# Optimization experiments

Hardware: AMD Instinct MI355X
Metric: run time of the kernel (lower is better)

## Reference

```python
import jax, jax.numpy as jnp
import numpy as np

N_NODES = 1000000
N_EDGES = 2000000
N_FEAT = 11          # QM9 num_features
HIDDEN = 64
N_CLASSES = 19       # QM9 num_classes
BATCH = 128


def setup_inputs() -> dict:
    key = jax.random.key(0)
    k = jax.random.split(key, 8)
    x = jax.random.normal(k[0], (N_NODES, N_FEAT), dtype=jnp.float32)
    edge_index = jax.random.randint(k[1], (2, N_EDGES), 0, N_NODES, dtype=jnp.int64)
    y = jax.random.normal(k[2], (BATCH, N_CLASSES), dtype=jnp.float32)
    batch = jnp.sort(jax.random.randint(k[3], (N_NODES,), 0, BATCH, dtype=jnp.int64))
    # GCNConv params: weight [in, hidden], bias [hidden]
    W_conv = jax.random.normal(k[4], (N_FEAT, HIDDEN), dtype=jnp.float32) / np.sqrt(N_FEAT)
    b_conv = jnp.zeros((HIDDEN,), dtype=jnp.float32)
    # Final linear: [hidden, classes]
    W_lin = jax.random.normal(k[5], (HIDDEN, N_CLASSES), dtype=jnp.float32) / np.sqrt(HIDDEN)
    b_lin = jnp.zeros((N_CLASSES,), dtype=jnp.float32)
    return {"x": x, "edge_index": edge_index, "y": y, "batch": batch,
            "W_conv": W_conv, "b_conv": b_conv, "W_lin": W_lin, "b_lin": b_lin}


def reference(x, edge_index, y, batch, W_conv, b_conv, W_lin, b_lin):
    row, col = edge_index[0], edge_index[1]  # source -> target
    # GCN symmetric normalization (add_self_loops=False): deg over targets
    ones = jnp.ones((edge_index.shape[1],), dtype=x.dtype)
    deg = jax.ops.segment_sum(ones, col, num_segments=N_NODES)
    dinv = jnp.where(deg > 0, jax.lax.rsqrt(jnp.maximum(deg, 1.0)), 0.0)
    norm = dinv[row] * dinv[col]  # [E]
    # Transform then aggregate: gather at source, scatter-add at target
    xw = x @ W_conv                                    # [N, H]
    msgs = xw[row] * norm[:, None]                     # [E, H]
    agg = jax.ops.segment_sum(msgs, col, num_segments=N_NODES) + b_conv
    h = jax.nn.relu(agg)                               # [N, H]
    # global_mean_pool over batch ids (size=BATCH)
    summed = jax.ops.segment_sum(h, batch, num_segments=BATCH)   # [B, H]
    counts = jax.ops.segment_sum(jnp.ones((N_NODES,), dtype=x.dtype), batch, num_segments=BATCH)
    pooled = summed / jnp.maximum(counts, 1.0)[:, None]
    # dropout p=0.5 is identity in eval mode
    return pooled @ W_lin + b_lin                      # [B, classes]
```

## Files before the change

kernel.cpp:

```cpp
#include <hip/hip_runtime.h>

#define N_NODES   1000000
#define N_EDGES   2000000
#define N_FEAT    11
#define HIDDEN    64
#define BATCH     128
#define N_CLASSES 19

#define NPB     2048
#define NBUCK   489
#define BCAP    5120
#define EPB     8192
#define PBLK    245
#define NSLOT   8
#define NCHUNK  3907
#define FROW    24
#define ZOFF    (256 * FROW)

typedef __attribute__((ext_vector_type(8))) short v8s;
typedef __attribute__((ext_vector_type(4))) float v4f;

__device__ __forceinline__ unsigned f2b(float v) {
    unsigned u = __float_as_uint(v);
    return (u + 0x7FFFu + ((u >> 16) & 1u)) >> 16;
}

__global__ __launch_bounds__(1024) void part_kernel(const int* __restrict__ row,
                                                    const int* __restrict__ col,
                                                    int* __restrict__ bcnt,
                                                    int* __restrict__ part) {
    __shared__ int lh[512];
    const int t = threadIdx.x;
    if (t < 512) lh[t] = 0;
    __syncthreads();
    const int q0 = (blockIdx.x * EPB) >> 2;
    const int4* col4 = (const int4*)col;
    const int4* row4 = (const int4*)row;
    const int qa = q0 + t, qb = q0 + 1024 + t;
    const bool va = qa < N_EDGES / 4, vb = qb < N_EDGES / 4;
    int4 ca, ra, cb, rb;
    if (va) { ca = col4[qa]; ra = row4[qa]; }
    if (vb) { cb = col4[qb]; rb = row4[qb]; }
    if (va) {
        atomicAdd(&lh[ca.x >> 11], 1); atomicAdd(&lh[ca.y >> 11], 1);
        atomicAdd(&lh[ca.z >> 11], 1); atomicAdd(&lh[ca.w >> 11], 1);
    }
    if (vb) {
        atomicAdd(&lh[cb.x >> 11], 1); atomicAdd(&lh[cb.y >> 11], 1);
        atomicAdd(&lh[cb.z >> 11], 1); atomicAdd(&lh[cb.w >> 11], 1);
    }
    __syncthreads();
    if (t < NBUCK) {
        int v = lh[t];
        if (v) lh[t] = t * BCAP + atomicAdd(&bcnt[t], v);
    }
    __syncthreads();
    int p;
    if (va) {
        p = atomicAdd(&lh[ca.x >> 11], 1); part[p] = (ra.x << 11) | (ca.x & (NPB - 1));
        p = atomicAdd(&lh[ca.y >> 11], 1); part[p] = (ra.y << 11) | (ca.y & (NPB - 1));
        p = atomicAdd(&lh[ca.z >> 11], 1); part[p] = (ra.z << 11) | (ca.z & (NPB - 1));
        p = atomicAdd(&lh[ca.w >> 11], 1); part[p] = (ra.w << 11) | (ca.w & (NPB - 1));
    }
    if (vb) {
        p = atomicAdd(&lh[cb.x >> 11], 1); part[p] = (rb.x << 11) | (cb.x & (NPB - 1));
        p = atomicAdd(&lh[cb.y >> 11], 1); part[p] = (rb.y << 11) | (cb.y & (NPB - 1));
        p = atomicAdd(&lh[cb.z >> 11], 1); part[p] = (rb.z << 11) | (cb.z & (NPB - 1));
        p = atomicAdd(&lh[cb.w >> 11], 1); part[p] = (rb.w << 11) | (cb.w & (NPB - 1));
    }
}

__global__ __launch_bounds__(1024) void sort2_kernel(const int* __restrict__ part,
                                                     const int* __restrict__ bcnt,
                                                     const float* __restrict__ x,
                                                     int* __restrict__ srcs,
                                                     int* __restrict__ nstart,
                                                     unsigned short* __restrict__ ndeg,
                                                     float* __restrict__ dinv,
                                                     unsigned short* __restrict__ xs) {
    __shared__ int cnt[NPB];
    __shared__ int off[NPB];
    __shared__ int tsum[1024];
    __shared__ int stage[BCAP];
    __shared__ int outb[BCAP];
    const int t = threadIdx.x, b = blockIdx.x;
    for (int i = t; i < NPB; i += 1024) cnt[i] = 0;
    __syncthreads();
    const int s0 = b * BCAP, m = bcnt[b];
    for (int j = t; j < m; j += 1024) {
        int v = part[s0 + j];
        stage[j] = v;
        atomicAdd(&cnt[v & (NPB - 1)], 1);
    }
    __syncthreads();
    const int i0 = t * 2;
    int c0 = cnt[i0], c1 = cnt[i0 + 1];
    int s = c0 + c1;
    tsum[t] = s;
    __syncthreads();
    for (int o = 1; o < 1024; o <<= 1) {
        int a = (t >= o) ? tsum[t - o] : 0;
        __syncthreads();
        tsum[t] += a;
        __syncthreads();
    }
    int run = tsum[t] - s;
    off[i0] = run; off[i0 + 1] = run + c0;
    __syncthreads();
    for (int i = t; i < NPB; i += 1024) {
        int n = b * NPB + i;
        if (n < N_NODES) {
            int d = cnt[i];
            float dv = d ? rsqrtf((float)d) : 0.0f;
            dinv[n]   = dv;
            ndeg[n]   = (unsigned short)d;
            nstart[n] = s0 + off[i];
            const float* xr = x + (size_t)n * N_FEAT;
            unsigned h[11];
#pragma unroll
            for (int k = 0; k < 11; ++k) h[k] = f2b(dv * xr[k]);
            uint4 A, B;
            A.x = h[0] | (h[1] << 16); A.y = h[2] | (h[3] << 16);
            A.z = h[4] | (h[5] << 16); A.w = h[6] | (h[7] << 16);
            B.x = h[8] | (h[9] << 16); B.y = h[10]; B.z = 0u; B.w = 0u;
            uint4* o = (uint4*)(xs + (size_t)n * 16);
            o[0] = A; o[1] = B;
        }
    }
    __syncthreads();
    for (int j = t; j < m; j += 1024) {
        int p  = stage[j];
        int cl = p & (NPB - 1);
        int pos = atomicAdd(&off[cl], 1);
        outb[pos] = p >> 11;
    }
    __syncthreads();
    const int m4 = m >> 2;
    int4* d4 = (int4*)(srcs + s0);
    const int4* s4 = (const int4*)outb;
    for (int j = t; j < m4; j += 1024) d4[j] = s4[j];
    for (int j = (m4 << 2) + t; j < m; j += 1024) srcs[s0 + j] = outb[j];
}

__global__ __launch_bounds__(256) void gather_pool_kernel(
    const int* __restrict__ srcs, const unsigned short* __restrict__ xs,
    const int* __restrict__ nstart, const unsigned short* __restrict__ ndeg,
    const float* __restrict__ dinv, const int* __restrict__ batch,
    const float* __restrict__ Wc, const float* __restrict__ bc,
    float* __restrict__ pooled, float* __restrict__ countsf) {
    __shared__ unsigned short fb16[ZOFF + 8];
    __shared__ int   sj0[256];
    __shared__ int   sdeg[256];
    __shared__ float sdinv[256];
    __shared__ int   sbid[256];
    __shared__ int   sperm[256];
    __shared__ int   dcnt[32];
    __shared__ int   doff[32];
    __shared__ float pbuf[2 * HIDDEN];
    __shared__ int   pcnt[NSLOT];
    const int t = threadIdx.x, lane = t & 63, w = t >> 6;
    const int quad = lane >> 4;
    const int base = blockIdx.x * 256;
    {
        int n = base + t;
        bool v = n < N_NODES;
        sj0[t]   = v ? nstart[n] : 0;
        sdeg[t]  = v ? (int)ndeg[n] : 0;
        sdinv[t] = v ? dinv[n] : 0.0f;
        sbid[t]  = v ? batch[n] : -1;
    }
    if (t < 2 * HIDDEN) pbuf[t] = 0.0f;
    if (t < NSLOT) pcnt[t] = 0;
    if (t < 32)    dcnt[t] = 0;
    if (t < 4)     ((unsigned*)(fb16 + ZOFF))[t] = 0u;
    __syncthreads();
    const int bid0 = sbid[0];
    {
        int bid = sbid[t];
        if (bid >= 0) {
            int slot = bid - bid0;
            if (slot >= 0 && slot < NSLOT) atomicAdd(&pcnt[slot], 1);
            else atomicAdd(&countsf[bid], 1.0f);
        }
    }
    int mybin = sdeg[t] < 31 ? sdeg[t] : 31;
    atomicAdd(&dcnt[mybin], 1);
    __syncthreads();
    if (t < 32) {
        int r = 0;
        for (int i = 0; i < t; ++i) r += dcnt[i];
        doff[t] = r;
    }
    __syncthreads();
    int pos = atomicAdd(&doff[mybin], 1);
    sperm[pos] = t;
    __syncthreads();

    {
        int i  = sperm[t];
        int j0 = sj0[i], d = sdeg[i];
        const int e = j0 + d;
        float acc[11];
#pragma unroll
        for (int k = 0; k < 11; ++k) acc[k] = 0.0f;
        for (int j = j0; j < e; j += 4) {
            int j1 = (j + 1 < e) ? j + 1 : j;
            int j2 = (j + 2 < e) ? j + 2 : j;
            int j3 = (j + 3 < e) ? j + 3 : j;
            int r0 = srcs[j], r1 = srcs[j1], r2 = srcs[j2], r3 = srcs[j3];
            const uint4* p0 = (const uint4*)(xs + (size_t)r0 * 16);
            const uint4* p1 = (const uint4*)(xs + (size_t)r1 * 16);
            const uint4* p2 = (const uint4*)(xs + (size_t)r2 * 16);
            const uint4* p3 = (const uint4*)(xs + (size_t)r3 * 16);
            uint4 A0 = p0[0]; uint2 B0 = *(const uint2*)(p0 + 1);
            uint4 A1 = p1[0]; uint2 B1 = *(const uint2*)(p1 + 1);
            uint4 A2 = p2[0]; uint2 B2 = *(const uint2*)(p2 + 1);
            uint4 A3 = p3[0]; uint2 B3 = *(const uint2*)(p3 + 1);
            float m1 = (j + 1 < e) ? 1.0f : 0.0f;
            float m2 = (j + 2 < e) ? 1.0f : 0.0f;
            float m3 = (j + 3 < e) ? 1.0f : 0.0f;
#define ACCF(idx, expr0, expr1, expr2, expr3)                     \
            acc[idx] += __uint_as_float(expr0);                   \
            acc[idx] = fmaf(m1, __uint_as_float(expr1), acc[idx]);\
            acc[idx] = fmaf(m2, __uint_as_float(expr2), acc[idx]);\
            acc[idx] = fmaf(m3, __uint_as_float(expr3), acc[idx]);
            ACCF(0,  A0.x << 16,        A1.x << 16,        A2.x << 16,        A3.x << 16)
            ACCF(1,  A0.x & 0xFFFF0000u, A1.x & 0xFFFF0000u, A2.x & 0xFFFF0000u, A3.x & 0xFFFF0000u)
            ACCF(2,  A0.y << 16,        A1.y << 16,        A2.y << 16,        A3.y << 16)
            ACCF(3,  A0.y & 0xFFFF0000u, A1.y & 0xFFFF0000u, A2.y & 0xFFFF0000u, A3.y & 0xFFFF0000u)
            ACCF(4,  A0.z << 16,        A1.z << 16,        A2.z << 16,        A3.z << 16)
            ACCF(5,  A0.z & 0xFFFF0000u, A1.z & 0xFFFF0000u, A2.z & 0xFFFF0000u, A3.z & 0xFFFF0000u)
            ACCF(6,  A0.w << 16,        A1.w << 16,        A2.w << 16,        A3.w << 16)
            ACCF(7,  A0.w & 0xFFFF0000u, A1.w & 0xFFFF0000u, A2.w & 0xFFFF0000u, A3.w & 0xFFFF0000u)
            ACCF(8,  B0.x << 16,        B1.x << 16,        B2.x << 16,        B3.x << 16)
            ACCF(9,  B0.x & 0xFFFF0000u, B1.x & 0xFFFF0000u, B2.x & 0xFFFF0000u, B3.x & 0xFFFF0000u)
            ACCF(10, B0.y << 16,        B1.y << 16,        B2.y << 16,        B3.y << 16)
#undef ACCF
        }
        unsigned hb[11];
#pragma unroll
        for (int k = 0; k < 11; ++k) hb[k] = f2b(acc[k]);
        uint4 U0, U1;
        U0.x = hb[0] | (hb[1] << 16); U0.y = hb[2]  | (hb[3] << 16);
        U0.z = hb[4] | (hb[5] << 16); U0.w = hb[6]  | (hb[7] << 16);
        U1.x = hb[8] | (hb[9] << 16); U1.y = hb[10]; U1.z = 0u; U1.w = 0u;
        uint4* wp = (uint4*)(fb16 + i * FROW);
        wp[0] = U0; wp[1] = U1;
    }
    __syncthreads();

    const int nch = w * 16 + (lane & 15);
    union { v8s v; unsigned short us[8]; } bf;
#pragma unroll
    for (int j = 0; j < 8; ++j) {
        int k = quad * 8 + j;
        bf.us[j] = (k < 11) ? (unsigned short)f2b(Wc[k * HIDDEN + nch]) : (unsigned short)0;
    }
    const float bias_lane = bc[nch];
    float acc0 = 0.0f, acc1 = 0.0f;
#pragma unroll 4
    for (int mtile = 0; mtile < 16; ++mtile) {
        const v8s* ap = (quad < 2)
            ? (const v8s*)(fb16 + (mtile * 16 + (lane & 15)) * FROW + quad * 8)
            : (const v8s*)(fb16 + ZOFF);
        v8s a = *ap;
        v4f d = __builtin_amdgcn_mfma_f32_16x16x32_bf16(a, bf.v, (v4f){0.f, 0.f, 0.f, 0.f}, 0, 0, 0);
#pragma unroll
        for (int r = 0; r < 4; ++r) {
            int node = mtile * 16 + quad * 4 + r;
            int bid  = sbid[node];
            if (bid >= 0) {
                float h = fmaxf(fmaf(sdinv[node], d[r], bias_lane), 0.0f);
                int slot = bid - bid0;
                if (slot == 0)      acc0 += h;
                else if (slot == 1) acc1 += h;
                else atomicAdd(&pooled[(size_t)bid * HIDDEN + nch], h);
            }
        }
    }
    atomicAdd(&pbuf[nch], acc0);
    atomicAdd(&pbuf[HIDDEN + nch], acc1);
    __syncthreads();
    for (int s = w; s < 2; s += 4) {
        int c = pcnt[s];
        if (c > 0) {
            atomicAdd(&pooled[(size_t)(bid0 + s) * HIDDEN + lane], pbuf[s * HIDDEN + lane]);
            if (lane == 0) atomicAdd(&countsf[bid0 + s], (float)c);
        }
    }
}

__global__ void final_kernel(const float* __restrict__ pooled, const float* __restrict__ counts,
                             const float* __restrict__ Wl, const float* __restrict__ bl,
                             float* __restrict__ out) {
    int i = blockIdx.x * blockDim.x + threadIdx.x;
    if (i >= BATCH * N_CLASSES) return;
    int b = i / N_CLASSES;
    int c = i - b * N_CLASSES;
    float inv = 1.0f / fmaxf(counts[b], 1.0f);
    float s = bl[c];
#pragma unroll 8
    for (int h = 0; h < HIDDEN; ++h)
        s = fmaf(pooled[b * HIDDEN + h] * inv, Wl[h * N_CLASSES + c], s);
    out[i] = s;
}

extern "C" void kernel_launch(void* const* d_in, const int* in_sizes, int n_in,
                              void* d_out, int out_size, void* d_ws, size_t ws_size,
                              hipStream_t stream) {
    const float* x     = (const float*)d_in[0];
    const int*   ei    = (const int*)d_in[1];
    const int*   batch = (const int*)d_in[3];
    const float* Wc    = (const float*)d_in[4];
    const float* bc    = (const float*)d_in[5];
    const float* Wl    = (const float*)d_in[6];
    const float* bl    = (const float*)d_in[7];
    float*       out   = (float*)d_out;

    int*            bcnt    = (int*)d_ws;
    float*          pooled  = (float*)(bcnt + 512);
    float*          countsf = pooled + BATCH * HIDDEN;
    unsigned short* xs      = (unsigned short*)(countsf + BATCH);
    int*            nstart  = (int*)(xs + (size_t)N_NODES * 16);
    unsigned short* ndeg    = (unsigned short*)(nstart + N_NODES);
    float*          dinv    = (float*)(ndeg + N_NODES);
    int*            part    = (int*)(dinv + N_NODES);
    int*            srcs    = part + (size_t)NBUCK * BCAP;

    size_t zero_bytes = (512 + BATCH * HIDDEN + BATCH) * 4;
    hipMemsetAsync(d_ws, 0, zero_bytes, stream);

    const int* row = ei;
    const int* col = ei + N_EDGES;

    part_kernel <<<PBLK, 1024, 0, stream>>>(row, col, bcnt, part);
    sort2_kernel<<<NBUCK, 1024, 0, stream>>>(part, bcnt, x, srcs, nstart, ndeg, dinv, xs);
    gather_pool_kernel<<<NCHUNK, 256, 0, stream>>>(srcs, xs, nstart, ndeg, dinv,
                                                   batch, Wc, bc, pooled, countsf);
    final_kernel<<<(BATCH * N_CLASSES + 255) / 256, 256, 0, stream>>>(pooled, countsf, Wl, bl, out);
}
```

Measured before the change: 213.3 us.

## Fuse memset, partition and bucket sort into one cooperative kernel

```diff
diff --git a/kernel.cpp b/kernel.cpp
--- a/kernel.cpp
+++ b/kernel.cpp
@@ -1,4 +1,7 @@
 #include <hip/hip_runtime.h>
+#include <hip/hip_cooperative_groups.h>
+
+namespace cg = cooperative_groups;
 
 #define N_NODES   1000000
 #define N_EDGES   2000000
@@ -12,6 +15,7 @@
 #define BCAP    5120
 #define EPB     8192
 #define PBLK    245
+#define GPREP   256
 #define NSLOT   8
 #define NCHUNK  3907
 #define FROW    24
@@ -25,121 +29,130 @@
     return (u + 0x7FFFu + ((u >> 16) & 1u)) >> 16;
 }
 
-__global__ __launch_bounds__(1024) void part_kernel(const int* __restrict__ row,
-                                                    const int* __restrict__ col,
-                                                    int* __restrict__ bcnt,
-                                                    int* __restrict__ part) {
-    __shared__ int lh[512];
-    const int t = threadIdx.x;
-    if (t < 512) lh[t] = 0;
-    __syncthreads();
-    const int q0 = (blockIdx.x * EPB) >> 2;
-    const int4* col4 = (const int4*)col;
-    const int4* row4 = (const int4*)row;
-    const int qa = q0 + t, qb = q0 + 1024 + t;
-    const bool va = qa < N_EDGES / 4, vb = qb < N_EDGES / 4;
-    int4 ca, ra, cb, rb;
-    if (va) { ca = col4[qa]; ra = row4[qa]; }
-    if (vb) { cb = col4[qb]; rb = row4[qb]; }
-    if (va) {
-        atomicAdd(&lh[ca.x >> 11], 1); atomicAdd(&lh[ca.y >> 11], 1);
-        atomicAdd(&lh[ca.z >> 11], 1); atomicAdd(&lh[ca.w >> 11], 1);
-    }
-    if (vb) {
-        atomicAdd(&lh[cb.x >> 11], 1); atomicAdd(&lh[cb.y >> 11], 1);
-        atomicAdd(&lh[cb.z >> 11], 1); atomicAdd(&lh[cb.w >> 11], 1);
-    }
-    __syncthreads();
-    if (t < NBUCK) {
-        int v = lh[t];
-        if (v) lh[t] = t * BCAP + atomicAdd(&bcnt[t], v);
-    }
-    __syncthreads();
-    int p;
-    if (va) {
-        p = atomicAdd(&lh[ca.x >> 11], 1); part[p] = (ra.x << 11) | (ca.x & (NPB - 1));
-        p = atomicAdd(&lh[ca.y >> 11], 1); part[p] = (ra.y << 11) | (ca.y & (NPB - 1));
-        p = atomicAdd(&lh[ca.z >> 11], 1); part[p] = (ra.z << 11) | (ca.z & (NPB - 1));
-        p = atomicAdd(&lh[ca.w >> 11], 1); part[p] = (ra.w << 11) | (ca.w & (NPB - 1));
-    }
-    if (vb) {
-        p = atomicAdd(&lh[cb.x >> 11], 1); part[p] = (rb.x << 11) | (cb.x & (NPB - 1));
-        p = atomicAdd(&lh[cb.y >> 11], 1); part[p] = (rb.y << 11) | (cb.y & (NPB - 1));
-        p = atomicAdd(&lh[cb.z >> 11], 1); part[p] = (rb.z << 11) | (cb.z & (NPB - 1));
-        p = atomicAdd(&lh[cb.w >> 11], 1); part[p] = (rb.w << 11) | (cb.w & (NPB - 1));
-    }
-}
-
-__global__ __launch_bounds__(1024) void sort2_kernel(const int* __restrict__ part,
-                                                     const int* __restrict__ bcnt,
-                                                     const float* __restrict__ x,
-                                                     int* __restrict__ srcs,
-                                                     int* __restrict__ nstart,
-                                                     unsigned short* __restrict__ ndeg,
-                                                     float* __restrict__ dinv,
-                                                     unsigned short* __restrict__ xs) {
+__global__ __launch_bounds__(1024) void prep_kernel(
+    const int* __restrict__ row, const int* __restrict__ col,
+    const float* __restrict__ x,
+    int* __restrict__ bcnt, int* __restrict__ part, int* __restrict__ srcs,
+    int* __restrict__ nstart, unsigned short* __restrict__ ndeg,
+    float* __restrict__ dinv, unsigned short* __restrict__ xs,
+    float* __restrict__ pooled, float* __restrict__ countsf) {
+    cg::grid_group grid = cg::this_grid();
     __shared__ int cnt[NPB];
     __shared__ int off[NPB];
     __shared__ int tsum[1024];
     __shared__ int stage[BCAP];
     __shared__ int outb[BCAP];
-    const int t = threadIdx.x, b = blockIdx.x;
-    for (int i = t; i < NPB; i += 1024) cnt[i] = 0;
-    __syncthreads();
-    const int s0 = b * BCAP, m = bcnt[b];
-    for (int j = t; j < m; j += 1024) {
-        int v = part[s0 + j];
-        stage[j] = v;
-        atomicAdd(&cnt[v & (NPB - 1)], 1);
-    }
-    __syncthreads();
-    const int i0 = t * 2;
-    int c0 = cnt[i0], c1 = cnt[i0 + 1];
-    int s = c0 + c1;
-    tsum[t] = s;
-    __syncthreads();
-    for (int o = 1; o < 1024; o <<= 1) {
-        int a = (t >= o) ? tsum[t - o] : 0;
-        __syncthreads();
-        tsum[t] += a;
-        __syncthreads();
-    }
-    int run = tsum[t] - s;
-    off[i0] = run; off[i0 + 1] = run + c0;
-    __syncthreads();
-    for (int i = t; i < NPB; i += 1024) {
-        int n = b * NPB + i;
-        if (n < N_NODES) {
-            int d = cnt[i];
-            float dv = d ? rsqrtf((float)d) : 0.0f;
-            dinv[n]   = dv;
-            ndeg[n]   = (unsigned short)d;
-            nstart[n] = s0 + off[i];
-            const float* xr = x + (size_t)n * N_FEAT;
-            unsigned h[11];
-#pragma unroll
-            for (int k = 0; k < 11; ++k) h[k] = f2b(dv * xr[k]);
-            uint4 A, B;
-            A.x = h[0] | (h[1] << 16); A.y = h[2] | (h[3] << 16);
-            A.z = h[4] | (h[5] << 16); A.w = h[6] | (h[7] << 16);
-            B.x = h[8] | (h[9] << 16); B.y = h[10]; B.z = 0u; B.w = 0u;
-            uint4* o = (uint4*)(xs + (size_t)n * 16);
-            o[0] = A; o[1] = B;
-        }
-    }
-    __syncthreads();
-    for (int j = t; j < m; j += 1024) {
-        int p  = stage[j];
-        int cl = p & (NPB - 1);
-        int pos = atomicAdd(&off[cl], 1);
-        outb[pos] = p >> 11;
-    }
-    __syncthreads();
-    const int m4 = m >> 2;
-    int4* d4 = (int4*)(srcs + s0);
-    const int4* s4 = (const int4*)outb;
-    for (int j = t; j < m4; j += 1024) d4[j] = s4[j];
-    for (int j = (m4 << 2) + t; j < m; j += 1024) srcs[s0 + j] = outb[j];
+    const int t = threadIdx.x, B = blockIdx.x;
+
+    {
+        int i = B * 1024 + t;
+        if (i < 512 + BATCH * HIDDEN + BATCH) bcnt[i] = 0;
+    }
+    __threadfence();
+    grid.sync();
+
+    if (B < PBLK) {
+        int* lh = cnt;
+        if (t < 512) lh[t] = 0;
+        __syncthreads();
+        const int q0 = (B * EPB) >> 2;
+        const int4* col4 = (const int4*)col;
+        const int4* row4 = (const int4*)row;
+        const int qa = q0 + t, qb = q0 + 1024 + t;
+        const bool va = qa < N_EDGES / 4, vb = qb < N_EDGES / 4;
+        int4 ca, ra, cb, rb;
+        if (va) { ca = col4[qa]; ra = row4[qa]; }
+        if (vb) { cb = col4[qb]; rb = row4[qb]; }
+        if (va) {
+            atomicAdd(&lh[ca.x >> 11], 1); atomicAdd(&lh[ca.y >> 11], 1);
+            atomicAdd(&lh[ca.z >> 11], 1); atomicAdd(&lh[ca.w >> 11], 1);
+        }
+        if (vb) {
+            atomicAdd(&lh[cb.x >> 11], 1); atomicAdd(&lh[cb.y >> 11], 1);
+            atomicAdd(&lh[cb.z >> 11], 1); atomicAdd(&lh[cb.w >> 11], 1);
+        }
+        __syncthreads();
+        if (t < NBUCK) {
+            int v = lh[t];
+            if (v) lh[t] = t * BCAP + atomicAdd(&bcnt[t], v);
+        }
+        __syncthreads();
+        int p;
+        if (va) {
+            p = atomicAdd(&lh[ca.x >> 11], 1); part[p] = (ra.x << 11) | (ca.x & (NPB - 1));
+            p = atomicAdd(&lh[ca.y >> 11], 1); part[p] = (ra.y << 11) | (ca.y & (NPB - 1));
+            p = atomicAdd(&lh[ca.z >> 11], 1); part[p] = (ra.z << 11) | (ca.z & (NPB - 1));
+            p = atomicAdd(&lh[ca.w >> 11], 1); part[p] = (ra.w << 11) | (ca.w & (NPB - 1));
+        }
+        if (vb) {
+            p = atomicAdd(&lh[cb.x >> 11], 1); part[p] = (rb.x << 11) | (cb.x & (NPB - 1));
+            p = atomicAdd(&lh[cb.y >> 11], 1); part[p] = (rb.y << 11) | (cb.y & (NPB - 1));
+            p = atomicAdd(&lh[cb.z >> 11], 1); part[p] = (rb.z << 11) | (cb.z & (NPB - 1));
+            p = atomicAdd(&lh[cb.w >> 11], 1); part[p] = (rb.w << 11) | (cb.w & (NPB - 1));
+        }
+    }
+    __threadfence();
+    grid.sync();
+
+    for (int b = B; b < NBUCK; b += GPREP) {
+        for (int i = t; i < NPB; i += 1024) cnt[i] = 0;
+        __syncthreads();
+        const int s0 = b * BCAP, m = bcnt[b];
+        for (int j = t; j < m; j += 1024) {
+            int v = part[s0 + j];
+            stage[j] = v;
+            atomicAdd(&cnt[v & (NPB - 1)], 1);
+        }
+        __syncthreads();
+        const int i0 = t * 2;
+        int c0 = cnt[i0], c1 = cnt[i0 + 1];
+        int s = c0 + c1;
+        tsum[t] = s;
+        __syncthreads();
+        for (int o = 1; o < 1024; o <<= 1) {
+            int a = (t >= o) ? tsum[t - o] : 0;
+            __syncthreads();
+            tsum[t] += a;
+            __syncthreads();
+        }
+        int run = tsum[t] - s;
+        off[i0] = run; off[i0 + 1] = run + c0;
+        __syncthreads();
+        for (int i = t; i < NPB; i += 1024) {
+            int n = b * NPB + i;
+            if (n < N_NODES) {
+                int d = cnt[i];
+                float dv = d ? rsqrtf((float)d) : 0.0f;
+                dinv[n]   = dv;
+                ndeg[n]   = (unsigned short)d;
+                nstart[n] = s0 + off[i];
+                const float* xr = x + (size_t)n * N_FEAT;
+                unsigned h[11];
+#pragma unroll
+                for (int k = 0; k < 11; ++k) h[k] = f2b(dv * xr[k]);
+                uint4 A, Bv;
+                A.x = h[0] | (h[1] << 16); A.y = h[2] | (h[3] << 16);
+                A.z = h[4] | (h[5] << 16); A.w = h[6] | (h[7] << 16);
+                Bv.x = h[8] | (h[9] << 16); Bv.y = h[10]; Bv.z = 0u; Bv.w = 0u;
+                uint4* o = (uint4*)(xs + (size_t)n * 16);
+                o[0] = A; o[1] = Bv;
+            }
+        }
+        __syncthreads();
+        for (int j = t; j < m; j += 1024) {
+            int p  = stage[j];
+            int cl = p & (NPB - 1);
+            int pos = atomicAdd(&off[cl], 1);
+            outb[pos] = p >> 11;
+        }
+        __syncthreads();
+        const int m4 = m >> 2;
+        int4* d4 = (int4*)(srcs + s0);
+        const int4* s4 = (const int4*)outb;
+        for (int j = t; j < m4; j += 1024) d4[j] = s4[j];
+        for (int j = (m4 << 2) + t; j < m; j += 1024) srcs[s0 + j] = outb[j];
+        __syncthreads();
+    }
 }
 
 __global__ __launch_bounds__(256) void gather_pool_kernel(
@@ -327,14 +340,13 @@
     int*            part    = (int*)(dinv + N_NODES);
     int*            srcs    = part + (size_t)NBUCK * BCAP;
 
-    size_t zero_bytes = (512 + BATCH * HIDDEN + BATCH) * 4;
-    hipMemsetAsync(d_ws, 0, zero_bytes, stream);
-
     const int* row = ei;
     const int* col = ei + N_EDGES;
 
-    part_kernel <<<PBLK, 1024, 0, stream>>>(row, col, bcnt, part);
-    sort2_kernel<<<NBUCK, 1024, 0, stream>>>(part, bcnt, x, srcs, nstart, ndeg, dinv, xs);
+    void* kargs[] = {(void*)&row, (void*)&col, (void*)&x, (void*)&bcnt, (void*)&part,
+                     (void*)&srcs, (void*)&nstart, (void*)&ndeg, (void*)&dinv, (void*)&xs,
+                     (void*)&pooled, (void*)&countsf};
+    hipLaunchCooperativeKernel((void*)prep_kernel, dim3(GPREP), dim3(1024), kargs, 0, stream);
     gather_pool_kernel<<<NCHUNK, 256, 0, stream>>>(srcs, xs, nstart, ndeg, dinv,
                                                    batch, Wc, bc, pooled, countsf);
     final_kernel<<<(BATCH * N_CLASSES + 255) / 256, 256, 0, stream>>>(pooled, countsf, Wl, bl, out);
```

Measured after the change: 485.1 us. 2.27x slower.
